# Kernel optimization log

Hardware: AMD Instinct MI355X
Metric: run time of the kernel (lower is better)

The kernel has to match this reference:

```python
import jax, jax.numpy as jnp
import numpy as np

IN_F, HID, OUT, NN = 64, 128, 64, 128
TOTAL = 4096  # 32 graphs * 128 nodes


def setup_inputs() -> dict:
    key = jax.random.key(0)
    ks = jax.random.split(key, 8)
    d_in = 1 + 2 * IN_F
    s1 = 1.0 / np.sqrt(d_in)
    s2 = 1.0 / np.sqrt(HID)
    return {
        "feat": jax.random.normal(ks[0], (TOTAL, IN_F), jnp.float32),
        "coordinate": jax.random.normal(ks[1], (TOTAL, 3), jnp.float32),
        "W1": jax.random.uniform(ks[2], (d_in, HID), jnp.float32, -s1, s1),
        "b1": jax.random.uniform(ks[3], (HID,), jnp.float32, -s1, s1),
        "W2": jax.random.uniform(ks[4], (HID, HID), jnp.float32, -s2, s2),
        "b2": jax.random.uniform(ks[5], (HID,), jnp.float32, -s2, s2),
        "W3": jax.random.uniform(ks[6], (HID, OUT), jnp.float32, -s2, s2),
        "b3": jax.random.uniform(ks[7], (OUT,), jnp.float32, -s2, s2),
        "num_nodes": NN,
    }


def reference(feat, coordinate, W1, b1, W2, b2, W3, b3, num_nodes):
    N = num_nodes
    B = feat.shape[0] // N
    h = feat.reshape(B, N, -1)        # [B,N,F]
    x = coordinate.reshape(B, N, -1)  # [B,N,3]
    # pairwise squared distance: [B,N,N,1]
    d2 = jnp.sum((x[:, None, :, :] - x[:, :, None, :]) ** 2, axis=-1, keepdims=True)
    F = h.shape[-1]
    # feat concat order matches torch: [h_j broadcast over dim1, h_i broadcast over dim2]
    hj = jnp.broadcast_to(h[:, None, :, :], (B, N, N, F))
    hi = jnp.broadcast_to(h[:, :, None, :], (B, N, N, F))
    z = jnp.concatenate([d2, hj, hi], axis=-1)  # [B,N,N,1+2F]
    z = jax.nn.silu(z @ W1 + b1)
    z = jax.nn.silu(z @ W2 + b2)
    z = z @ W3 + b3                   # [B,N,N,OUT]
    return jnp.sum(z, axis=(1, 2))    # [B,OUT]
```

## Files before the change

### kernel.cpp

```cpp
#include <hip/hip_runtime.h>
#include <hip/hip_bf16.h>

#define F_IN 64
#define HID 128
#define OUTF 64
#define NN 128
#define NB 32
#define TOTAL 4096

#define NEG_LOG2E (-1.4426950408889634f)
#define NEG_LN2 (-0.6931471805599453f)

typedef short bf16x8 __attribute__((ext_vector_type(8)));
typedef float f32x4 __attribute__((ext_vector_type(4)));

static __device__ __forceinline__ short f2bf(float v) {
  __hip_bfloat16 h = __float2bfloat16(v);
  return __builtin_bit_cast(short, h);
}

static __device__ __forceinline__ float fexp2(float x) {
#if __has_builtin(__builtin_amdgcn_exp2f)
  return __builtin_amdgcn_exp2f(x);
#else
  return exp2f(x);
#endif
}

__global__ __launch_bounds__(256) void uv_prep(
    const float* __restrict__ feat,
    const float* __restrict__ W1,
    const float* __restrict__ W2,
    const float* __restrict__ b1,
    const float* __restrict__ b2,
    float* __restrict__ uvp,
    __hip_bfloat16* __restrict__ w2swz,
    float* __restrict__ w0p,
    float* __restrict__ b2p) {
  __shared__ __align__(16) char wcat[256 * 128];
  const int tid = threadIdx.x;
  {
    const int c = tid;
    const int cc = c & 127;
    const int rbase = (c < HID) ? 1 : 65;
#pragma unroll
    for (int p = 0; p < 8; ++p) {
      bf16x8 pk;
#pragma unroll
      for (int m = 0; m < 8; ++m)
        pk[m] = f2bf(W1[(rbase + p * 8 + m) * HID + cc]);
      *reinterpret_cast<bf16x8*>(wcat + c * 128 + ((p ^ (c & 7)) << 4)) = pk;
    }
  }
  if (blockIdx.x < 64) {
    const int e = blockIdx.x * 256 + tid;
    const int kk = e >> 7, cc2 = e & 127;
    const int byo = cc2 * 256 + (((kk >> 3) ^ (cc2 & 7)) << 4) + (kk & 7) * 2;
    *reinterpret_cast<__hip_bfloat16*>(reinterpret_cast<char*>(w2swz) + byo) =
        __float2bfloat16(W2[kk * HID + cc2]);
  } else if (blockIdx.x == 64) {
    if (tid < HID) w0p[tid] = NEG_LOG2E * W1[tid];
    else b2p[tid - HID] = NEG_LOG2E * b2[tid - HID];
  }
  __syncthreads();

  const int wave = tid >> 6, lane = tid & 63;
  const int lr = lane & 15, kg = lane >> 4;
  const int r0 = blockIdx.x * 16;

  f32x4 acc[4];
#pragma unroll
  for (int ct = 0; ct < 4; ++ct) acc[ct] = {0.f, 0.f, 0.f, 0.f};

#pragma unroll
  for (int ks = 0; ks < 2; ++ks) {
    const float* fp = feat + (size_t)(r0 + lr) * F_IN + ks * 32 + kg * 8;
    const f32x4 fa = *reinterpret_cast<const f32x4*>(fp);
    const f32x4 fb = *reinterpret_cast<const f32x4*>(fp + 4);
    bf16x8 a;
#pragma unroll
    for (int m = 0; m < 4; ++m) {
      a[m] = f2bf(fa[m]);
      a[4 + m] = f2bf(fb[m]);
    }
    const int slot = ks * 4 + kg;
#pragma unroll
    for (int ct = 0; ct < 4; ++ct) {
      const int c = wave * 64 + ct * 16 + lr;
      const bf16x8 w = *reinterpret_cast<const bf16x8*>(
          wcat + c * 128 + ((slot ^ (c & 7)) << 4));
      acc[ct] = __builtin_amdgcn_mfma_f32_16x16x32_bf16(a, w, acc[ct], 0, 0, 0);
    }
  }
#pragma unroll
  for (int ct = 0; ct < 4; ++ct) {
    const int c = wave * 64 + ct * 16 + lr;
    const float badd = (c >= HID) ? b1[c - HID] : 0.f;
#pragma unroll
    for (int reg = 0; reg < 4; ++reg) {
      const int r = r0 + kg * 4 + reg;
      uvp[(size_t)r * 256 + c] = NEG_LOG2E * (acc[ct][reg] + badd);
    }
  }
}

__global__ __launch_bounds__(256, 3) void sake_main(
    const float* __restrict__ coord,
    const float* __restrict__ w0p,
    const float* __restrict__ b2p,
    const float* __restrict__ uvp,
    const __hip_bfloat16* __restrict__ w2swz,
    float* __restrict__ part) {
  __shared__ __align__(16) char w2lds[HID * 256];
  __shared__ float ssum[4][HID];

  const int tid = threadIdx.x;
  const int bid = (blockIdx.x & 7) * 512 + (blockIdx.x >> 3);
  const int b = bid >> 7, i = bid & 127;

  {
    const char* src = reinterpret_cast<const char*>(w2swz);
#pragma unroll
    for (int p = 0; p < 8; ++p) {
      const int o = tid * 16 + p * 4096;
      *reinterpret_cast<int4*>(w2lds + o) =
          *reinterpret_cast<const int4*>(src + o);
    }
  }

  const int wave = tid >> 6, lane = tid & 63;
  const int lr = lane & 15, kg = lane >> 4;
  const int j0 = wave * 32;

  const float* urow0 = uvp + ((size_t)b * NN + j0 + lr) * 256;
  const float* urow1 = urow0 + 16 * 256;
  const float* vrow = uvp + ((size_t)b * NN + i) * 256 + HID;

  f32x4 uA0 = *reinterpret_cast<const f32x4*>(urow0 + kg * 8);
  f32x4 uA1 = *reinterpret_cast<const f32x4*>(urow0 + kg * 8 + 4);
  f32x4 uA2 = *reinterpret_cast<const f32x4*>(urow1 + kg * 8);
  f32x4 uA3 = *reinterpret_cast<const f32x4*>(urow1 + kg * 8 + 4);

  const float* xi = coord + (size_t)(b * NN + i) * 3;
  const float xix = xi[0], xiy = xi[1], xiz = xi[2];
  float d2t[2];
#pragma unroll
  for (int t = 0; t < 2; ++t) {
    const float* xj = coord + (size_t)(b * NN + j0 + t * 16 + lr) * 3;
    const float dx = xj[0] - xix, dy = xj[1] - xiy, dz = xj[2] - xiz;
    d2t[t] = dx * dx + dy * dy + dz * dz;
  }

  f32x4 acc[2][8];
#pragma unroll
  for (int c = 0; c < 8; ++c) {
    const float bb = b2p[c * 16 + lr];
    acc[0][c] = {bb, bb, bb, bb};
    acc[1][c] = {bb, bb, bb, bb};
  }

  __syncthreads();

#pragma unroll
  for (int ks = 0; ks < 4; ++ks) {
    f32x4 uB0, uB1, uB2, uB3;
    if (ks < 3) {
      const int cn = (ks + 1) * 32 + kg * 8;
      uB0 = *reinterpret_cast<const f32x4*>(urow0 + cn);
      uB1 = *reinterpret_cast<const f32x4*>(urow0 + cn + 4);
      uB2 = *reinterpret_cast<const f32x4*>(urow1 + cn);
      uB3 = *reinterpret_cast<const f32x4*>(urow1 + cn + 4);
    }
    const int c0 = ks * 32 + kg * 8;
    const f32x4 v0 = *reinterpret_cast<const f32x4*>(vrow + c0);
    const f32x4 v1 = *reinterpret_cast<const f32x4*>(vrow + c0 + 4);
    const f32x4 w0 = *reinterpret_cast<const f32x4*>(w0p + c0);
    const f32x4 w1 = *reinterpret_cast<const f32x4*>(w0p + c0 + 4);

    bf16x8 zb[2];
#pragma unroll
    for (int m = 0; m < 4; ++m) {
      const float z = fmaf(d2t[0], w0[m], uA0[m] + v0[m]);
      zb[0][m] = f2bf(z * __builtin_amdgcn_rcpf(1.f + fexp2(z)));
    }
#pragma unroll
    for (int m = 0; m < 4; ++m) {
      const float z = fmaf(d2t[0], w1[m], uA1[m] + v1[m]);
      zb[0][4 + m] = f2bf(z * __builtin_amdgcn_rcpf(1.f + fexp2(z)));
    }
#pragma unroll
    for (int m = 0; m < 4; ++m) {
      const float z = fmaf(d2t[1], w0[m], uA2[m] + v0[m]);
      zb[1][m] = f2bf(z * __builtin_amdgcn_rcpf(1.f + fexp2(z)));
    }
#pragma unroll
    for (int m = 0; m < 4; ++m) {
      const float z = fmaf(d2t[1], w1[m], uA3[m] + v1[m]);
      zb[1][4 + m] = f2bf(z * __builtin_amdgcn_rcpf(1.f + fexp2(z)));
    }

    const int rbase = lr * 256 + ((((ks << 2) | kg) ^ (lr & 7)) << 4);
    bf16x8 wf[4];
#pragma unroll
    for (int c = 0; c < 4; ++c)
      wf[c] = *reinterpret_cast<const bf16x8*>(w2lds + rbase + c * 4096);
#pragma unroll
    for (int c = 0; c < 4; ++c) {
      acc[0][c] = __builtin_amdgcn_mfma_f32_16x16x32_bf16(zb[0], wf[c], acc[0][c], 0, 0, 0);
      acc[1][c] = __builtin_amdgcn_mfma_f32_16x16x32_bf16(zb[1], wf[c], acc[1][c], 0, 0, 0);
    }
#pragma unroll
    for (int c = 0; c < 4; ++c)
      wf[c] = *reinterpret_cast<const bf16x8*>(w2lds + rbase + (4 + c) * 4096);
#pragma unroll
    for (int c = 0; c < 4; ++c) {
      acc[0][4 + c] = __builtin_amdgcn_mfma_f32_16x16x32_bf16(zb[0], wf[c], acc[0][4 + c], 0, 0, 0);
      acc[1][4 + c] = __builtin_amdgcn_mfma_f32_16x16x32_bf16(zb[1], wf[c], acc[1][4 + c], 0, 0, 0);
    }

    uA0 = uB0; uA1 = uB1; uA2 = uB2; uA3 = uB3;
  }

#pragma unroll
  for (int c = 0; c < 8; ++c) {
    float s = 0.f;
#pragma unroll
    for (int t = 0; t < 2; ++t)
#pragma unroll
      for (int m = 0; m < 4; ++m) {
        const float z = acc[t][c][m];
        s = fmaf(z, __builtin_amdgcn_rcpf(1.f + fexp2(z)), s);
      }
    s += __shfl_xor(s, 16);
    s += __shfl_xor(s, 32);
    acc[0][c][0] = s;
  }
  if (lane < 16) {
#pragma unroll
    for (int c = 0; c < 8; ++c) ssum[wave][c * 16 + lane] = acc[0][c][0];
  }
  __syncthreads();
  if (tid < HID) {
    part[(size_t)bid * HID + tid] =
        ssum[0][tid] + ssum[1][tid] + ssum[2][tid] + ssum[3][tid];
  }
}

__global__ void final_kernel(const float* __restrict__ part,
                             const float* __restrict__ W3,
                             const float* __restrict__ b3,
                             float* __restrict__ out) {
  __shared__ float s2[2][HID];
  __shared__ float s[HID];
  int b = blockIdx.x, t = threadIdx.x;
  int c = t & 127, half = t >> 7;
  float a = 0.f;
  for (int g = half * 64; g < half * 64 + 64; ++g)
    a += part[(size_t)(b * NN + g) * HID + c];
  s2[half][c] = a;
  __syncthreads();
  if (t < HID) s[t] = (s2[0][t] + s2[1][t]) * NEG_LN2;
  __syncthreads();
  if (t < OUTF) {
    float o = 16384.f * b3[t];
    for (int c2 = 0; c2 < HID; ++c2) o += s[c2] * W3[c2 * OUTF + t];
    out[b * OUTF + t] = o;
  }
}

extern "C" void kernel_launch(void* const* d_in, const int* in_sizes, int n_in,
                              void* d_out, int out_size, void* d_ws, size_t ws_size,
                              hipStream_t stream) {
  const float* feat = (const float*)d_in[0];
  const float* coord = (const float*)d_in[1];
  const float* W1 = (const float*)d_in[2];
  const float* b1 = (const float*)d_in[3];
  const float* W2 = (const float*)d_in[4];
  const float* b2 = (const float*)d_in[5];
  const float* W3 = (const float*)d_in[6];
  const float* b3 = (const float*)d_in[7];
  float* out = (float*)d_out;

  char* ws = (char*)d_ws;
  __hip_bfloat16* w2swz = (__hip_bfloat16*)ws;
  float* w0p = (float*)(ws + 32 * 1024);
  float* b2p = (float*)(ws + 36 * 1024);
  float* uvp = (float*)(ws + 64 * 1024);
  float* part = (float*)(ws + 64 * 1024 + 4096 * 1024);

  uv_prep<<<256, 256, 0, stream>>>(feat, W1, W2, b1, b2, uvp, w2swz, w0p, b2p);
  sake_main<<<TOTAL, 256, 0, stream>>>(coord, w0p, b2p, uvp, w2swz, part);
  final_kernel<<<NB, 256, 0, stream>>>(part, W3, b3, out);
}
```

Measured before the change: 60.24 us.

## Process four i-rows per block to amortize W2 LDS staging

Each block of sake_main now handles four consecutive i nodes in a loop instead of one, cutting the grid from 4096 to 1024 blocks. The 32 KB W2 copy into LDS, the j coordinates and the bias loads are done once per block and reused across the four rows, with per-column silu sums kept in registers across iterations. The final reduction kernel is changed to sum 32 partials per graph instead of 128. The cost is fewer blocks for latency hiding, and the u-row prefetch across k-steps is gone, so each k-step now waits on its own global loads.

```diff
diff --git a/kernel.cpp b/kernel.cpp
--- a/kernel.cpp
+++ b/kernel.cpp
@@ -115,8 +115,9 @@
   __shared__ float ssum[4][HID];
 
   const int tid = threadIdx.x;
-  const int bid = (blockIdx.x & 7) * 512 + (blockIdx.x >> 3);
-  const int b = bid >> 7, i = bid & 127;
+  const int bid = (blockIdx.x & 7) * 128 + (blockIdx.x >> 3);
+  const int b = bid >> 5;
+  const int ig = bid & 31;
 
   {
     const char* src = reinterpret_cast<const char*>(w2swz);
@@ -134,110 +135,118 @@
 
   const float* urow0 = uvp + ((size_t)b * NN + j0 + lr) * 256;
   const float* urow1 = urow0 + 16 * 256;
-  const float* vrow = uvp + ((size_t)b * NN + i) * 256 + HID;
-
-  f32x4 uA0 = *reinterpret_cast<const f32x4*>(urow0 + kg * 8);
-  f32x4 uA1 = *reinterpret_cast<const f32x4*>(urow0 + kg * 8 + 4);
-  f32x4 uA2 = *reinterpret_cast<const f32x4*>(urow1 + kg * 8);
-  f32x4 uA3 = *reinterpret_cast<const f32x4*>(urow1 + kg * 8 + 4);
-
-  const float* xi = coord + (size_t)(b * NN + i) * 3;
-  const float xix = xi[0], xiy = xi[1], xiz = xi[2];
-  float d2t[2];
-#pragma unroll
-  for (int t = 0; t < 2; ++t) {
-    const float* xj = coord + (size_t)(b * NN + j0 + t * 16 + lr) * 3;
-    const float dx = xj[0] - xix, dy = xj[1] - xiy, dz = xj[2] - xiz;
-    d2t[t] = dx * dx + dy * dy + dz * dz;
-  }
-
-  f32x4 acc[2][8];
+
+  const float* xj0 = coord + (size_t)(b * NN + j0 + lr) * 3;
+  const float* xj1 = coord + (size_t)(b * NN + j0 + 16 + lr) * 3;
+  const float xj0x = xj0[0], xj0y = xj0[1], xj0z = xj0[2];
+  const float xj1x = xj1[0], xj1y = xj1[1], xj1z = xj1[2];
+
+  float bb[8];
+#pragma unroll
+  for (int c = 0; c < 8; ++c) bb[c] = b2p[c * 16 + lr];
+
+  float csum[8];
+#pragma unroll
+  for (int c = 0; c < 8; ++c) csum[c] = 0.f;
+
+  __syncthreads();
+
+#pragma unroll 1
+  for (int it = 0; it < 4; ++it) {
+    const int i = ig * 4 + it;
+    const float* xip = coord + (size_t)(b * NN + i) * 3;
+    const float xix = xip[0], xiy = xip[1], xiz = xip[2];
+    float d2t[2];
+    {
+      const float dx = xj0x - xix, dy = xj0y - xiy, dz = xj0z - xiz;
+      d2t[0] = dx * dx + dy * dy + dz * dz;
+      const float ex = xj1x - xix, ey = xj1y - xiy, ez = xj1z - xiz;
+      d2t[1] = ex * ex + ey * ey + ez * ez;
+    }
+    const float* vrow = uvp + ((size_t)b * NN + i) * 256 + HID;
+
+    f32x4 acc[2][8];
+#pragma unroll
+    for (int c = 0; c < 8; ++c) {
+      acc[0][c] = {bb[c], bb[c], bb[c], bb[c]};
+      acc[1][c] = {bb[c], bb[c], bb[c], bb[c]};
+    }
+
+#pragma unroll
+    for (int ks = 0; ks < 4; ++ks) {
+      const int c0 = ks * 32 + kg * 8;
+      const f32x4 uA0 = *reinterpret_cast<const f32x4*>(urow0 + c0);
+      const f32x4 uA1 = *reinterpret_cast<const f32x4*>(urow0 + c0 + 4);
+      const f32x4 uA2 = *reinterpret_cast<const f32x4*>(urow1 + c0);
+      const f32x4 uA3 = *reinterpret_cast<const f32x4*>(urow1 + c0 + 4);
+      const f32x4 v0 = *reinterpret_cast<const f32x4*>(vrow + c0);
+      const f32x4 v1 = *reinterpret_cast<const f32x4*>(vrow + c0 + 4);
+      const f32x4 w0 = *reinterpret_cast<const f32x4*>(w0p + c0);
+      const f32x4 w1 = *reinterpret_cast<const f32x4*>(w0p + c0 + 4);
+
+      bf16x8 zb[2];
+#pragma unroll
+      for (int m = 0; m < 4; ++m) {
+        const float z = fmaf(d2t[0], w0[m], uA0[m] + v0[m]);
+        zb[0][m] = f2bf(z * __builtin_amdgcn_rcpf(1.f + fexp2(z)));
+      }
+#pragma unroll
+      for (int m = 0; m < 4; ++m) {
+        const float z = fmaf(d2t[0], w1[m], uA1[m] + v1[m]);
+        zb[0][4 + m] = f2bf(z * __builtin_amdgcn_rcpf(1.f + fexp2(z)));
+      }
+#pragma unroll
+      for (int m = 0; m < 4; ++m) {
+        const float z = fmaf(d2t[1], w0[m], uA2[m] + v0[m]);
+        zb[1][m] = f2bf(z * __builtin_amdgcn_rcpf(1.f + fexp2(z)));
+      }
+#pragma unroll
+      for (int m = 0; m < 4; ++m) {
+        const float z = fmaf(d2t[1], w1[m], uA3[m] + v1[m]);
+        zb[1][4 + m] = f2bf(z * __builtin_amdgcn_rcpf(1.f + fexp2(z)));
+      }
+
+      const int rbase = lr * 256 + ((((ks << 2) | kg) ^ (lr & 7)) << 4);
+      bf16x8 wf[4];
+#pragma unroll
+      for (int c = 0; c < 4; ++c)
+        wf[c] = *reinterpret_cast<const bf16x8*>(w2lds + rbase + c * 4096);
+#pragma unroll
+      for (int c = 0; c < 4; ++c) {
+        acc[0][c] = __builtin_amdgcn_mfma_f32_16x16x32_bf16(zb[0], wf[c], acc[0][c], 0, 0, 0);
+        acc[1][c] = __builtin_amdgcn_mfma_f32_16x16x32_bf16(zb[1], wf[c], acc[1][c], 0, 0, 0);
+      }
+#pragma unroll
+      for (int c = 0; c < 4; ++c)
+        wf[c] = *reinterpret_cast<const bf16x8*>(w2lds + rbase + (4 + c) * 4096);
+#pragma unroll
+      for (int c = 0; c < 4; ++c) {
+        acc[0][4 + c] = __builtin_amdgcn_mfma_f32_16x16x32_bf16(zb[0], wf[c], acc[0][4 + c], 0, 0, 0);
+        acc[1][4 + c] = __builtin_amdgcn_mfma_f32_16x16x32_bf16(zb[1], wf[c], acc[1][4 + c], 0, 0, 0);
+      }
+    }
+
+#pragma unroll
+    for (int c = 0; c < 8; ++c)
+#pragma unroll
+      for (int t = 0; t < 2; ++t)
+#pragma unroll
+        for (int m = 0; m < 4; ++m) {
+          const float z = acc[t][c][m];
+          csum[c] = fmaf(z, __builtin_amdgcn_rcpf(1.f + fexp2(z)), csum[c]);
+        }
+  }
+
 #pragma unroll
   for (int c = 0; c < 8; ++c) {
-    const float bb = b2p[c * 16 + lr];
-    acc[0][c] = {bb, bb, bb, bb};
-    acc[1][c] = {bb, bb, bb, bb};
-  }
-
-  __syncthreads();
-
-#pragma unroll
-  for (int ks = 0; ks < 4; ++ks) {
-    f32x4 uB0, uB1, uB2, uB3;
-    if (ks < 3) {
-      const int cn = (ks + 1) * 32 + kg * 8;
-      uB0 = *reinterpret_cast<const f32x4*>(urow0 + cn);
-      uB1 = *reinterpret_cast<const f32x4*>(urow0 + cn + 4);
-      uB2 = *reinterpret_cast<const f32x4*>(urow1 + cn);
-      uB3 = *reinterpret_cast<const f32x4*>(urow1 + cn + 4);
-    }
-    const int c0 = ks * 32 + kg * 8;
-    const f32x4 v0 = *reinterpret_cast<const f32x4*>(vrow + c0);
-    const f32x4 v1 = *reinterpret_cast<const f32x4*>(vrow + c0 + 4);
-    const f32x4 w0 = *reinterpret_cast<const f32x4*>(w0p + c0);
-    const f32x4 w1 = *reinterpret_cast<const f32x4*>(w0p + c0 + 4);
-
-    bf16x8 zb[2];
-#pragma unroll
-    for (int m = 0; m < 4; ++m) {
-      const float z = fmaf(d2t[0], w0[m], uA0[m] + v0[m]);
-      zb[0][m] = f2bf(z * __builtin_amdgcn_rcpf(1.f + fexp2(z)));
-    }
-#pragma unroll
-    for (int m = 0; m < 4; ++m) {
-      const float z = fmaf(d2t[0], w1[m], uA1[m] + v1[m]);
-      zb[0][4 + m] = f2bf(z * __builtin_amdgcn_rcpf(1.f + fexp2(z)));
-    }
-#pragma unroll
-    for (int m = 0; m < 4; ++m) {
-      const float z = fmaf(d2t[1], w0[m], uA2[m] + v0[m]);
-      zb[1][m] = f2bf(z * __builtin_amdgcn_rcpf(1.f + fexp2(z)));
-    }
-#pragma unroll
-    for (int m = 0; m < 4; ++m) {
-      const float z = fmaf(d2t[1], w1[m], uA3[m] + v1[m]);
-      zb[1][4 + m] = f2bf(z * __builtin_amdgcn_rcpf(1.f + fexp2(z)));
-    }
-
-    const int rbase = lr * 256 + ((((ks << 2) | kg) ^ (lr & 7)) << 4);
-    bf16x8 wf[4];
-#pragma unroll
-    for (int c = 0; c < 4; ++c)
-      wf[c] = *reinterpret_cast<const bf16x8*>(w2lds + rbase + c * 4096);
-#pragma unroll
-    for (int c = 0; c < 4; ++c) {
-      acc[0][c] = __builtin_amdgcn_mfma_f32_16x16x32_bf16(zb[0], wf[c], acc[0][c], 0, 0, 0);
-      acc[1][c] = __builtin_amdgcn_mfma_f32_16x16x32_bf16(zb[1], wf[c], acc[1][c], 0, 0, 0);
-    }
-#pragma unroll
-    for (int c = 0; c < 4; ++c)
-      wf[c] = *reinterpret_cast<const bf16x8*>(w2lds + rbase + (4 + c) * 4096);
-#pragma unroll
-    for (int c = 0; c < 4; ++c) {
-      acc[0][4 + c] = __builtin_amdgcn_mfma_f32_16x16x32_bf16(zb[0], wf[c], acc[0][4 + c], 0, 0, 0);
-      acc[1][4 + c] = __builtin_amdgcn_mfma_f32_16x16x32_bf16(zb[1], wf[c], acc[1][4 + c], 0, 0, 0);
-    }
-
-    uA0 = uB0; uA1 = uB1; uA2 = uB2; uA3 = uB3;
-  }
-
-#pragma unroll
-  for (int c = 0; c < 8; ++c) {
-    float s = 0.f;
-#pragma unroll
-    for (int t = 0; t < 2; ++t)
-#pragma unroll
-      for (int m = 0; m < 4; ++m) {
-        const float z = acc[t][c][m];
-        s = fmaf(z, __builtin_amdgcn_rcpf(1.f + fexp2(z)), s);
-      }
+    float s = csum[c];
     s += __shfl_xor(s, 16);
     s += __shfl_xor(s, 32);
-    acc[0][c][0] = s;
+    csum[c] = s;
   }
   if (lane < 16) {
 #pragma unroll
-    for (int c = 0; c < 8; ++c) ssum[wave][c * 16 + lane] = acc[0][c][0];
+    for (int c = 0; c < 8; ++c) ssum[wave][c * 16 + lane] = csum[c];
   }
   __syncthreads();
   if (tid < HID) {
@@ -255,8 +264,8 @@
   int b = blockIdx.x, t = threadIdx.x;
   int c = t & 127, half = t >> 7;
   float a = 0.f;
-  for (int g = half * 64; g < half * 64 + 64; ++g)
-    a += part[(size_t)(b * NN + g) * HID + c];
+  for (int g = half * 16; g < half * 16 + 16; ++g)
+    a += part[(size_t)(b * 32 + g) * HID + c];
   s2[half][c] = a;
   __syncthreads();
   if (t < HID) s[t] = (s2[0][t] + s2[1][t]) * NEG_LN2;
@@ -289,6 +298,6 @@
   float* part = (float*)(ws + 64 * 1024 + 4096 * 1024);
 
   uv_prep<<<256, 256, 0, stream>>>(feat, W1, W2, b1, b2, uvp, w2swz, w0p, b2p);
-  sake_main<<<TOTAL, 256, 0, stream>>>(coord, w0p, b2p, uvp, w2swz, part);
+  sake_main<<<1024, 256, 0, stream>>>(coord, w0p, b2p, uvp, w2swz, part);
   final_kernel<<<NB, 256, 0, stream>>>(part, W3, b3, out);
 }
```

After: 215.3 us. 257% more time.
